# Kernel tuning notes

Measured on AMD Instinct MI355X. Metric: run time of the kernel, lower is better.

## Reference

```python
import jax, jax.numpy as jnp
import numpy as np

N, D_IN, D_OUT, E, H = 2048, 1024, 256, 50, 256  # tokens, input_dim, output_dim, edge_nodes, expert hidden
RH = 512  # distributed_processor hidden


def setup_inputs() -> dict:
    key = jax.random.key(0)
    ks = jax.random.split(key, 16)
    w = lambda k, shape: jax.random.normal(k, shape, jnp.float32) * 0.02
    z = lambda *shape: jnp.zeros(shape, jnp.float32)
    return {
        "x": jax.random.normal(ks[0], (N, D_IN), jnp.float32),
        # 50 expert MLPs: Linear(D_IN,H)-ReLU-Linear(H,D_OUT), stacked over E
        "ew1": w(ks[1], (E, D_IN, H)), "eb1": z(E, H),
        "ew2": w(ks[2], (E, H, D_OUT)), "eb2": z(E, D_OUT),
        # distributed_processor: Linear(E*D_OUT,RH)-ReLU-Linear(RH,D_OUT)
        "dw1": w(ks[3], (E * D_OUT, RH)), "db1": z(RH),
        "dw2": w(ks[4], (RH, D_OUT)), "db2": z(D_OUT),
        # latency_optimizer: Linear(D_IN,256)-ReLU-Linear(256,1)-Sigmoid
        "lw1": w(ks[5], (D_IN, 256)), "lb1": z(256),
        "lw2": w(ks[6], (256, 1)), "lb2": z(1),
        # bandwidth_optimizer: same structure
        "bw1": w(ks[7], (D_IN, 256)), "bb1": z(256),
        "bw2": w(ks[8], (256, 1)), "bb2": z(1),
        # privacy_preserver: Linear(D_OUT,256)-ReLU-Linear(256,D_OUT)
        "pw1": w(ks[9], (D_OUT, 256)), "pb1": z(256),
        "pw2": w(ks[10], (256, D_OUT)), "pb2": z(D_OUT),
    }


def reference(x, ew1, eb1, ew2, eb2, dw1, db1, dw2, db2,
              lw1, lb1, lw2, lb2, bw1, bb1, bw2, bb2,
              pw1, pb1, pw2, pb2):
    n = x.shape[0]
    # grouped expert MLPs (replaces the Python for-loop over edge nodes)
    h = jax.nn.relu(jnp.einsum('ni,eih->neh', x, ew1) + eb1)        # [N,E,H]
    expert_out = jnp.einsum('neh,eho->neo', h, ew2) + eb2           # [N,E,D_OUT]
    cat = expert_out.reshape(n, E * D_OUT)                          # torch.cat(dim=-1)
    # distributed_processor reduce
    dist = jax.nn.relu(cat @ dw1 + db1) @ dw2 + db2                 # [N,D_OUT]
    # gating scalars
    lat = jax.nn.sigmoid(jax.nn.relu(x @ lw1 + lb1) @ lw2 + lb2)    # [N,1]
    bwd = jax.nn.sigmoid(jax.nn.relu(x @ bw1 + bb1) @ bw2 + bb2)    # [N,1]
    # privacy_preserver
    priv = jax.nn.relu(dist @ pw1 + pb1) @ pw2 + pb2                # [N,D_OUT]
    return priv * lat * bwd
```

## Files before the change

kernel.cpp:

```cpp
#include <hip/hip_runtime.h>
#include <hip/hip_bf16.h>

typedef unsigned short u16;
typedef __attribute__((ext_vector_type(8))) __bf16 v8bf;
typedef __attribute__((ext_vector_type(4))) float v4f;

#define DEVINL __device__ __forceinline__

DEVINL u16 f2bf(float f) {
  union { float f; unsigned u; } v; v.f = f;
  unsigned u = v.u;
  return (u16)((u + 0x7FFFu + ((u >> 16) & 1u)) >> 16);
}
DEVINL float bf2f(u16 b) {
  union { unsigned u; float f; } v; v.u = ((unsigned)b) << 16;
  return v.f;
}

DEVINL void async16(const void* g, void* l) {
  __builtin_amdgcn_global_load_lds(
      (__attribute__((address_space(1))) void*)(g),
      (__attribute__((address_space(3))) void*)(l), 16, 0, 0);
}

DEVINL void f2b_body(const float* __restrict__ src, u16* __restrict__ dst, int base) {
  int i = base + threadIdx.x * 4;
  float4 v = *(const float4*)(src + i);
  unsigned lo = (unsigned)f2bf(v.x) | ((unsigned)f2bf(v.y) << 16);
  unsigned hi = (unsigned)f2bf(v.z) | ((unsigned)f2bf(v.w) << 16);
  uint2 o; o.x = lo; o.y = hi;
  *(uint2*)(dst + i) = o;
}

DEVINL void tr64(u16 (*t)[66], const float* __restrict__ src,
                 u16* __restrict__ dst, int R, int C, int bx, int by) {
  int r0 = by * 64, c0 = bx * 64;
  int tx = threadIdx.x & 15, ty = threadIdx.x >> 4;
#pragma unroll
  for (int i = 0; i < 4; ++i) {
    int rr = ty + i * 16;
    float4 v = *(const float4*)(src + (long)(r0 + rr) * C + c0 + tx * 4);
    u16* d = &t[rr][tx * 4];
    d[0] = f2bf(v.x); d[1] = f2bf(v.y); d[2] = f2bf(v.z); d[3] = f2bf(v.w);
  }
  __syncthreads();
#pragma unroll
  for (int i = 0; i < 4; ++i) {
    int cc = ty + i * 16;
    ushort4 o;
    o.x = t[tx * 4 + 0][cc]; o.y = t[tx * 4 + 1][cc];
    o.z = t[tx * 4 + 2][cc]; o.w = t[tx * 4 + 3][cc];
    *(ushort4*)(dst + (long)(c0 + cc) * R + r0 + tx * 4) = o;
  }
}

__global__ __launch_bounds__(256) void k_prep(
    const float* __restrict__ x, const float* __restrict__ ew2,
    const float* __restrict__ ew1, const float* __restrict__ dw1,
    const float* __restrict__ dw2, const float* __restrict__ lw1,
    const float* __restrict__ bw1, const float* __restrict__ pw1,
    const float* __restrict__ pw2,
    const float* __restrict__ eb1, const float* __restrict__ lb1,
    const float* __restrict__ bb1,
    u16* __restrict__ xb, u16* __restrict__ ew2b, u16* __restrict__ ew1tf,
    u16* __restrict__ dw1t, u16* __restrict__ dw2t,
    u16* __restrict__ pw1t, u16* __restrict__ pw2t,
    float* __restrict__ ebcat) {
  __shared__ u16 tile[64][66];
  int b = blockIdx.x;
  if (b < 2048) { f2b_body(x, xb, b * 1024); return; }
  b -= 2048;
  if (b < 3200) { f2b_body(ew2, ew2b, b * 1024); return; }
  b -= 3200;
  if (b < 3200) {
    int e = b >> 6, t = b & 63;
    tr64(tile, ew1 + (long)e * 1024 * 256, ew1tf + (long)e * 256 * 1024,
         1024, 256, t & 3, t >> 2);
    return;
  }
  b -= 3200;
  if (b < 1600) {
    tr64(tile, dw1, dw1t, 12800, 512, b & 7, b >> 3);
    return;
  }
  b -= 1600;
  if (b < 32) {
    tr64(tile, dw2, dw2t, 512, 256, b & 3, b >> 2);
    return;
  }
  b -= 32;
  if (b < 64) {
    tr64(tile, lw1, ew1tf + (long)12800 * 1024, 1024, 256, b & 3, b >> 2);
    return;
  }
  b -= 64;
  if (b < 64) {
    tr64(tile, bw1, ew1tf + (long)13056 * 1024, 1024, 256, b & 3, b >> 2);
    return;
  }
  b -= 64;
  if (b < 16) {
    tr64(tile, pw1, pw1t, 256, 256, b & 3, b >> 2);
    return;
  }
  b -= 16;
  if (b < 16) {
    tr64(tile, pw2, pw2t, 256, 256, b & 3, b >> 2);
    return;
  }
  b -= 16;
  {
    int i = b * 256 + threadIdx.x;
    float v;
    if (i < 12800) v = eb1[i];
    else if (i < 13056) v = lb1[i - 12800];
    else v = bb1[i - 13056];
    ebcat[i] = v;
  }
}

DEVINL void gemm128_body(u16* __restrict__ sA, u16* __restrict__ sB,
    int bx, int by, int z,
    const u16* __restrict__ A, int lda, long aBatch,
    const u16* __restrict__ B, int ldb, long bBatch,
    void* __restrict__ Cp, int ldc, long cBatch,
    int K,
    const float* __restrict__ bias, long biasBatch,
    const float* __restrict__ rowscale, int flags) {
  const int tid = threadIdx.x;
  const int w = tid >> 6, l = tid & 63;
  const u16* Ab = A + (long)z * aBatch + (long)by * 128 * lda;
  const u16* Bb = B + (long)z * bBatch + (long)bx * 128 * ldb;
  const int ldaB = lda * 2, ldbB = ldb * 2;
  const int wm = w >> 1, wn = w & 1;
  const int r = l & 15, kq = l >> 4;

  const int f0 = w * 1024 + l * 16;
  const int f1 = f0 + 4096;
  const int row0 = f0 >> 6, cb0 = f0 & 63;
  const int row1 = f1 >> 6, cb1 = f1 & 63;
  const int seg0 = w * 1024, seg1 = seg0 + 4096;

  v4f acc[4][4];
#pragma unroll
  for (int m = 0; m < 4; ++m)
#pragma unroll
    for (int n = 0; n < 4; ++n) acc[m][n] = v4f{0.f, 0.f, 0.f, 0.f};

  const char* gA = (const char*)Ab;
  const char* gB = (const char*)Bb;
  const int nkt = K / 32;

  async16(gA + (long)row0 * ldaB + cb0, (char*)sA + seg0);
  async16(gA + (long)row1 * ldaB + cb1, (char*)sA + seg1);
  async16(gB + (long)row0 * ldbB + cb0, (char*)sB + seg0);
  async16(gB + (long)row1 * ldbB + cb1, (char*)sB + seg1);
  __syncthreads();

  for (int kt = 0; kt < nkt; ++kt) {
    const int cur = kt & 1;
    if (kt + 1 < nkt) {
      const long ko = (long)(kt + 1) * 64;
      async16(gA + ko + (long)row0 * ldaB + cb0, (char*)sA + (cur ^ 1) * 8192 + seg0);
      async16(gA + ko + (long)row1 * ldaB + cb1, (char*)sA + (cur ^ 1) * 8192 + seg1);
      async16(gB + ko + (long)row0 * ldbB + cb0, (char*)sB + (cur ^ 1) * 8192 + seg0);
      async16(gB + ko + (long)row1 * ldbB + cb1, (char*)sB + (cur ^ 1) * 8192 + seg1);
    }
    v8bf af[4], bfr[4];
#pragma unroll
    for (int m = 0; m < 4; ++m)
      af[m] = *(const v8bf*)&sA[cur * 4096 + (wm * 64 + m * 16 + r) * 32 + kq * 8];
#pragma unroll
    for (int n = 0; n < 4; ++n)
      bfr[n] = *(const v8bf*)&sB[cur * 4096 + (wn * 64 + n * 16 + r) * 32 + kq * 8];
#pragma unroll
    for (int m = 0; m < 4; ++m)
#pragma unroll
      for (int n = 0; n < 4; ++n)
        acc[m][n] = __builtin_amdgcn_mfma_f32_16x16x32_bf16(af[m], bfr[n], acc[m][n], 0, 0, 0);
    __syncthreads();
  }

  const float* bz = bias ? (bias + (long)z * biasBatch) : nullptr;
  const long rowBase = (long)by * 128 + wm * 64 + kq * 4;
  const int colBase = bx * 128 + wn * 64 + r;
  float* Cf = (float*)Cp + (long)z * cBatch;
  u16* Ch = (u16*)Cp + (long)z * cBatch;
#pragma unroll
  for (int m = 0; m < 4; ++m) {
#pragma unroll
    for (int n = 0; n < 4; ++n) {
      const int col = colBase + n * 16;
      const float bv = bz ? bz[col] : 0.f;
#pragma unroll
      for (int i = 0; i < 4; ++i) {
        const long row = rowBase + m * 16 + i;
        float v = acc[m][n][i] + bv;
        if (flags & 1) v = fmaxf(v, 0.f);
        if (rowscale) v *= rowscale[row];
        const long idx = row * ldc + col;
        if (flags & 2) Cf[idx] = v;
        else Ch[idx] = f2bf(v);
      }
    }
  }
}

__global__ __launch_bounds__(256) void k_gemm(
    const u16* __restrict__ A, int lda, long aBatch,
    const u16* __restrict__ B, int ldb, long bBatch,
    void* __restrict__ Cp, int ldc, long cBatch,
    int K,
    const float* __restrict__ bias, long biasBatch,
    const float* __restrict__ rowscale, int flags) {
  __shared__ __align__(16) u16 sA[2 * 4096];
  __shared__ __align__(16) u16 sB[2 * 4096];
  gemm128_body(sA, sB, blockIdx.x, blockIdx.y, blockIdx.z,
               A, lda, aBatch, B, ldb, bBatch, Cp, ldc, cBatch, K,
               bias, biasBatch, rowscale, flags);
}

__global__ __launch_bounds__(256) void k_wft_bias(
    const u16* __restrict__ dw1t, const u16* __restrict__ ew2b,
    u16* __restrict__ Wft,
    const float* __restrict__ eb2, const float* __restrict__ db1,
    float* __restrict__ biasf) {
  __shared__ __align__(16) u16 sA[2 * 4096];
  __shared__ __align__(16) u16 sB[2 * 4096];
  int b = blockIdx.x;
  if (b < 512) {
    const u16* row = dw1t + (long)b * 12800;
    float s = 0.f;
    for (int c = threadIdx.x; c < 1600; c += 256) {
      ushort4 a0 = *(const ushort4*)(row + c * 8);
      ushort4 a1 = *(const ushort4*)(row + c * 8 + 4);
      float4 e0 = *(const float4*)(eb2 + c * 8);
      float4 e1 = *(const float4*)(eb2 + c * 8 + 4);
      s += bf2f(a0.x) * e0.x + bf2f(a0.y) * e0.y + bf2f(a0.z) * e0.z + bf2f(a0.w) * e0.w
         + bf2f(a1.x) * e1.x + bf2f(a1.y) * e1.y + bf2f(a1.z) * e1.z + bf2f(a1.w) * e1.w;
    }
    float* red = (float*)sA;
    red[threadIdx.x] = s;
    __syncthreads();
    for (int off = 128; off > 0; off >>= 1) {
      if (threadIdx.x < off) red[threadIdx.x] += red[threadIdx.x + off];
      __syncthreads();
    }
    if (threadIdx.x == 0) biasf[b] = red[0] + db1[b];
    return;
  }
  b -= 512;
  int bx = b & 1, by = (b >> 1) & 3, z = b >> 3;
  gemm128_body(sA, sB, bx, by, z,
               dw1t, 12800, 256, ew2b, 256, (long)256 * 256,
               Wft, 12800, 256, 256, nullptr, 0, nullptr, 0);
}

#define LDS_T(buf, op) (smem + ((buf) * 2 + (op)) * 16384)

#define READ_A(buf, mh) do {                                                   \
  const char* _t = (const char*)LDS_T(buf, 0);                                 \
  _Pragma("unroll") for (int m = 0; m < 4; ++m)                                \
    _Pragma("unroll") for (int kk = 0; kk < 2; ++kk)                           \
      a[m][kk] = *(const v8bf*)(_t +                                           \
        (wm * 128 + (mh) * 64 + m * 16 + r15) * 128 +                          \
        ((kk * 64 + kq * 16) ^ (swr << 4)));                                   \
} while (0)

#define READ_B(buf, nh, br) do {                                               \
  const char* _t = (const char*)LDS_T(buf, 1);                                 \
  _Pragma("unroll") for (int n = 0; n < 2; ++n)                                \
    _Pragma("unroll") for (int kk = 0; kk < 2; ++kk)                           \
      br[n][kk] = *(const v8bf*)(_t +                                          \
        (wn * 64 + (nh) * 32 + n * 16 + r15) * 128 +                          \
        ((kk * 64 + kq * 16) ^ (swr << 4)));                                   \
} while (0)

#define MMA(mh, nh, br) do {                                                   \
  _Pragma("unroll") for (int kk = 0; kk < 2; ++kk)                             \
    _Pragma("unroll") for (int m = 0; m < 4; ++m)                              \
      _Pragma("unroll") for (int n = 0; n < 2; ++n)                            \
        acc[(mh) * 4 + m][(nh) * 2 + n] =                                      \
          __builtin_amdgcn_mfma_f32_16x16x32_bf16(                             \
            a[m][kk], br[n][kk], acc[(mh) * 4 + m][(nh) * 2 + n], 0, 0, 0);    \
} while (0)

#define BAR() __builtin_amdgcn_s_barrier()
#define PRIO1() __builtin_amdgcn_s_setprio(1)
#define PRIO0() __builtin_amdgcn_s_setprio(0)
#define VM6() asm volatile("s_waitcnt vmcnt(6)" ::: "memory")
#define VM0() asm volatile("s_waitcnt vmcnt(0)" ::: "memory")
#define LGKM0() asm volatile("s_waitcnt lgkmcnt(0)" ::: "memory")

__global__ __launch_bounds__(512, 2) void k_gemm256(
    const u16* __restrict__ A, int lda, long aBatch,
    const u16* __restrict__ B, int ldb, long bBatch,
    void* __restrict__ Cp, int ldc, long cBatch,
    int K, int NX,
    const float* __restrict__ bias,
    const float* __restrict__ rowscale, int flags) {
  __shared__ __align__(16) u16 smem[2 * 2 * 16384];

  const int lin = blockIdx.x;
  const int idx = (lin & 7) * NX + (lin >> 3);
  const int by = idx & 7, bx = idx >> 3;

  const int tid = threadIdx.x;
  const int w = tid >> 6, l = tid & 63;
  const int wm = w >> 2, wn = w & 3;
  const int r15 = l & 15, kq = l >> 4, swr = l & 7;
  const int z = blockIdx.z;

  const int rl = l >> 3;
  const int scol = ((l & 7) ^ rl) << 4;

  const long ldaB = (long)lda * 2, ldbB = (long)ldb * 2;
  const char* gAs = (const char*)(A + (long)z * aBatch) +
                    ((long)by * 256 + rl) * ldaB + scol;
  const char* gBs = (const char*)(B + (long)z * bBatch) +
                    ((long)bx * 256 + rl) * ldbB + scol;

  auto stA = [&](int buf, int R0, int kt) {
    async16(gAs + (long)R0 * ldaB + (long)kt * 128, (char*)LDS_T(buf, 0) + R0 * 128);
  };
  auto stB = [&](int buf, int R0, int kt) {
    async16(gBs + (long)R0 * ldbB + (long)kt * 128, (char*)LDS_T(buf, 1) + R0 * 128);
  };
  auto stAU0 = [&](int buf, int kt) { stA(buf, w * 8, kt);       stA(buf, 128 + w * 8, kt); };
  auto stAU1 = [&](int buf, int kt) { stA(buf, 64 + w * 8, kt);  stA(buf, 192 + w * 8, kt); };
  auto stBU0 = [&](int buf, int kt) { int R = (w >> 1) * 64 + (w & 1) * 16;      stB(buf, R, kt); stB(buf, R + 8, kt); };
  auto stBU1 = [&](int buf, int kt) { int R = (w >> 1) * 64 + (w & 1) * 16 + 32; stB(buf, R, kt); stB(buf, R + 8, kt); };

  v4f acc[8][4];
#pragma unroll
  for (int m = 0; m < 8; ++m)
#pragma unroll
    for (int n = 0; n < 4; ++n) acc[m][n] = v4f{0.f, 0.f, 0.f, 0.f};
  v8bf a[4][2], b0[2][2], b1[2][2];

  const int NT = K >> 6;
  const int NI = (NT >> 1) - 1;

  stAU0(0, 0); stBU0(0, 0); stBU1(0, 0); stAU1(0, 0);
  stAU0(1, 1); stBU0(1, 1); stBU1(1, 1);
  VM6();
  BAR();

  int kt0 = 0;
  for (int i = 0; i < NI; ++i, kt0 += 2) {
    READ_A(0, 0); READ_B(0, 0, b0);
    stAU1(1, kt0 + 1);
    BAR(); LGKM0(); PRIO1(); MMA(0, 0, b0); PRIO0(); BAR();
    READ_B(0, 1, b1);
    stAU0(0, kt0 + 2);
    BAR(); LGKM0(); PRIO1(); MMA(0, 1, b1); PRIO0(); BAR();
    READ_A(0, 1);
    stBU0(0, kt0 + 2);
    BAR(); LGKM0(); PRIO1(); MMA(1, 1, b1); PRIO0(); BAR();
    stBU1(0, kt0 + 2);
    BAR(); PRIO1(); MMA(1, 0, b0); PRIO0(); VM6(); BAR();
    READ_A(1, 0); READ_B(1, 0, b0);
    stAU1(0, kt0 + 2);
    BAR(); LGKM0(); PRIO1(); MMA(0, 0, b0); PRIO0(); BAR();
    READ_B(1, 1, b1);
    stAU0(1, kt0 + 3);
    BAR(); LGKM0(); PRIO1(); MMA(0, 1, b1); PRIO0(); BAR();
    READ_A(1, 1);
    stBU0(1, kt0 + 3);
    BAR(); LGKM0(); PRIO1(); MMA(1, 1, b1); PRIO0(); BAR();
    stBU1(1, kt0 + 3);
    BAR(); PRIO1(); MMA(1, 0, b0); PRIO0(); VM6(); BAR();
  }

  READ_A(0, 0); READ_B(0, 0, b0);
  stAU1(1, kt0 + 1);
  BAR(); LGKM0(); PRIO1(); MMA(0, 0, b0); PRIO0(); BAR();
  READ_B(0, 1, b1);
  BAR(); LGKM0(); PRIO1(); MMA(0, 1, b1); PRIO0(); BAR();
  READ_A(0, 1);
  BAR(); LGKM0(); PRIO1(); MMA(1, 1, b1); PRIO0(); BAR();
  BAR(); PRIO1(); MMA(1, 0, b0); PRIO0(); VM0(); BAR();
  READ_A(1, 0); READ_B(1, 0, b0);
  BAR(); LGKM0(); PRIO1(); MMA(0, 0, b0); PRIO0(); BAR();
  READ_B(1, 1, b1);
  BAR(); LGKM0(); PRIO1(); MMA(0, 1, b1); PRIO0(); BAR();
  READ_A(1, 1);
  BAR(); LGKM0(); PRIO1(); MMA(1, 1, b1); PRIO0(); BAR();
  PRIO1(); MMA(1, 0, b0); PRIO0();

  const long rowBase = (long)by * 256 + wm * 128 + kq * 4;
  const int colBase = bx * 256 + wn * 64 + r15;
  float* Cf = (float*)Cp + (long)z * cBatch;
  u16* Ch = (u16*)Cp + (long)z * cBatch;
#pragma unroll
  for (int mf = 0; mf < 8; ++mf) {
#pragma unroll
    for (int nf = 0; nf < 4; ++nf) {
      const int col = colBase + nf * 16;
      const float bv = bias ? bias[col] : 0.f;
#pragma unroll
      for (int j = 0; j < 4; ++j) {
        const long row = rowBase + mf * 16 + j;
        float v = acc[mf][nf][j] + bv;
        if (flags & 1) v = fmaxf(v, 0.f);
        if (rowscale) v *= rowscale[row];
        const long idx = row * ldc + col;
        if (flags & 2) Cf[idx] = v;
        else Ch[idx] = f2bf(v);
      }
    }
  }
}

__global__ __launch_bounds__(256) void k_tail(
    const float* __restrict__ part,
    const float* __restrict__ biasf,
    const u16* __restrict__ hg,
    const float* __restrict__ lw2, const float* __restrict__ lb2,
    const float* __restrict__ bw2, const float* __restrict__ bb2,
    const u16* __restrict__ dw2t,
    const float* __restrict__ db2,
    const u16* __restrict__ pw1t,
    const float* __restrict__ pb1,
    const u16* __restrict__ pw2t,
    const float* __restrict__ pb2,
    float* __restrict__ out) {
  __shared__ __align__(16) u16 dhs[16][520];
  __shared__ __align__(16) u16 ds2[16][264];
  __shared__ __align__(16) u16 phs[16][264];
  __shared__ float gl[16];
  const int tid = threadIdx.x;
  const int w = tid >> 6, l = tid & 63;
  const int r = l & 15, kq = l >> 4;
  const int r0 = blockIdx.x * 16;

#pragma unroll
  for (int i = 0; i < 8; ++i) {
    int e = (i * 256 + tid) * 4;
    int row = e >> 9, col = e & 511;
    const float* pp = part + (long)(r0 + row) * 512 + col;
    float4 s = *(const float4*)pp;
#pragma unroll
    for (int k = 1; k < 8; ++k) {
      float4 t = *(const float4*)(pp + (long)k * (2048 * 512));
      s.x += t.x; s.y += t.y; s.z += t.z; s.w += t.w;
    }
    float4 bv = *(const float4*)(biasf + col);
    ushort4 o;
    o.x = f2bf(fmaxf(s.x + bv.x, 0.f));
    o.y = f2bf(fmaxf(s.y + bv.y, 0.f));
    o.z = f2bf(fmaxf(s.z + bv.z, 0.f));
    o.w = f2bf(fmaxf(s.w + bv.w, 0.f));
    *(ushort4*)&dhs[row][col] = o;
  }

#pragma unroll
  for (int j = 0; j < 4; ++j) {
    int rr = w * 4 + j;
    const u16* rowp = hg + (long)(r0 + rr) * 13312;
    float sa = 0.f, sb = 0.f;
#pragma unroll
    for (int jj = 0; jj < 4; ++jj) {
      int i = l * 4 + jj;
      sa += bf2f(rowp[i]) * lw2[i];
      sb += bf2f(rowp[256 + i]) * bw2[i];
    }
#pragma unroll
    for (int off = 32; off > 0; off >>= 1) {
      sa += __shfl_down(sa, off, 64);
      sb += __shfl_down(sb, off, 64);
    }
    if (l == 0) {
      float ga = 1.f / (1.f + expf(-(sa + lb2[0])));
      float gb = 1.f / (1.f + expf(-(sb + bb2[0])));
      gl[rr] = ga * gb;
    }
  }
  __syncthreads();

  v4f acc[4];
#pragma unroll
  for (int n = 0; n < 4; ++n) acc[n] = v4f{0.f, 0.f, 0.f, 0.f};
#pragma unroll 4
  for (int kt = 0; kt < 16; ++kt) {
    v8bf af = *(const v8bf*)&dhs[r][kt * 32 + kq * 8];
#pragma unroll
    for (int n = 0; n < 4; ++n) {
      v8bf bf = *(const v8bf*)(dw2t + (long)(w * 64 + n * 16 + r) * 512 + kt * 32 + kq * 8);
      acc[n] = __builtin_amdgcn_mfma_f32_16x16x32_bf16(af, bf, acc[n], 0, 0, 0);
    }
  }
#pragma unroll
  for (int n = 0; n < 4; ++n) {
    int col = w * 64 + n * 16 + r;
    float bv = db2[col];
#pragma unroll
    for (int j = 0; j < 4; ++j) ds2[kq * 4 + j][col] = f2bf(acc[n][j] + bv);
  }
  __syncthreads();

#pragma unroll
  for (int n = 0; n < 4; ++n) acc[n] = v4f{0.f, 0.f, 0.f, 0.f};
#pragma unroll 4
  for (int kt = 0; kt < 8; ++kt) {
    v8bf af = *(const v8bf*)&ds2[r][kt * 32 + kq * 8];
#pragma unroll
    for (int n = 0; n < 4; ++n) {
      v8bf bf = *(const v8bf*)(pw1t + (long)(w * 64 + n * 16 + r) * 256 + kt * 32 + kq * 8);
      acc[n] = __builtin_amdgcn_mfma_f32_16x16x32_bf16(af, bf, acc[n], 0, 0, 0);
    }
  }
#pragma unroll
  for (int n = 0; n < 4; ++n) {
    int col = w * 64 + n * 16 + r;
    float bv = pb1[col];
#pragma unroll
    for (int j = 0; j < 4; ++j) phs[kq * 4 + j][col] = f2bf(fmaxf(acc[n][j] + bv, 0.f));
  }
  __syncthreads();

#pragma unroll
  for (int n = 0; n < 4; ++n) acc[n] = v4f{0.f, 0.f, 0.f, 0.f};
#pragma unroll 4
  for (int kt = 0; kt < 8; ++kt) {
    v8bf af = *(const v8bf*)&phs[r][kt * 32 + kq * 8];
#pragma unroll
    for (int n = 0; n < 4; ++n) {
      v8bf bf = *(const v8bf*)(pw2t + (long)(w * 64 + n * 16 + r) * 256 + kt * 32 + kq * 8);
      acc[n] = __builtin_amdgcn_mfma_f32_16x16x32_bf16(af, bf, acc[n], 0, 0, 0);
    }
  }
#pragma unroll
  for (int n = 0; n < 4; ++n) {
    int col = w * 64 + n * 16 + r;
    float bv = pb2[col];
#pragma unroll
    for (int j = 0; j < 4; ++j) {
      int row = kq * 4 + j;
      out[(long)(r0 + row) * 256 + col] = (acc[n][j] + bv) * gl[row];
    }
  }
}

extern "C" void kernel_launch(void* const* d_in, const int* in_sizes, int n_in,
                              void* d_out, int out_size, void* d_ws, size_t ws_size,
                              hipStream_t stream) {
  const float* x   = (const float*)d_in[0];
  const float* ew1 = (const float*)d_in[1];
  const float* eb1 = (const float*)d_in[2];
  const float* ew2 = (const float*)d_in[3];
  const float* eb2 = (const float*)d_in[4];
  const float* dw1 = (const float*)d_in[5];
  const float* db1 = (const float*)d_in[6];
  const float* dw2 = (const float*)d_in[7];
  const float* db2 = (const float*)d_in[8];
  const float* lw1 = (const float*)d_in[9];
  const float* lb1 = (const float*)d_in[10];
  const float* lw2 = (const float*)d_in[11];
  const float* lb2 = (const float*)d_in[12];
  const float* bw1 = (const float*)d_in[13];
  const float* bb1 = (const float*)d_in[14];
  const float* bw2 = (const float*)d_in[15];
  const float* bb2 = (const float*)d_in[16];
  const float* pw1 = (const float*)d_in[17];
  const float* pb1 = (const float*)d_in[18];
  const float* pw2 = (const float*)d_in[19];
  const float* pb2 = (const float*)d_in[20];

  const int S = 8, Ksplit = 1600;

  char* p = (char*)d_ws;
  auto alloc = [&](size_t bytes) {
    char* q = p;
    p += (bytes + 255) & ~(size_t)255;
    return q;
  };
  u16* xb      = (u16*)alloc((size_t)2048 * 1024 * 2);
  u16* ew1tf   = (u16*)alloc((size_t)13312 * 1024 * 2);
  u16* Wft     = (u16*)alloc((size_t)512 * 12800 * 2);
  u16* dw2t    = (u16*)alloc((size_t)256 * 512 * 2);
  u16* pw1t    = (u16*)alloc((size_t)256 * 256 * 2);
  u16* pw2t    = (u16*)alloc((size_t)256 * 256 * 2);
  float* ebcat = (float*)alloc(13312 * 4);
  float* biasf = (float*)alloc(512 * 4);
  float* part  = (float*)alloc((size_t)S * 2048 * 512 * 4);
  char* uni    = alloc((size_t)2048 * 13312 * 2);
  u16* h_all   = (u16*)uni;
  u16* ew2b    = (u16*)uni;
  u16* dw1t    = (u16*)(uni + (((size_t)50 * 256 * 256 * 2 + 255) & ~(size_t)255));
  (void)in_sizes; (void)n_in; (void)out_size; (void)ws_size;

  k_prep<<<dim3(10292), 256, 0, stream>>>(
      x, ew2, ew1, dw1, dw2, lw1, bw1, pw1, pw2, eb1, lb1, bb1,
      xb, ew2b, ew1tf, dw1t, dw2t, pw1t, pw2t, ebcat);

  k_wft_bias<<<dim3(912), 256, 0, stream>>>(dw1t, ew2b, Wft, eb2, db1, biasf);

  k_gemm256<<<dim3(416, 1, 1), 512, 0, stream>>>(
      xb, 1024, 0, ew1tf, 1024, 0, h_all, 13312, 0,
      1024, 52, ebcat, nullptr, 1);

  k_gemm<<<dim3(4, 16, S), 256, 0, stream>>>(
      h_all, 13312, Ksplit, Wft, 12800, Ksplit, part, 512, (long)2048 * 512,
      Ksplit, nullptr, 0, nullptr, 2);

  k_tail<<<dim3(128), 256, 0, stream>>>(
      part, biasf, h_all + 12800, lw2, lb2, bw2, bb2,
      dw2t, db2, pw1t, pb1, pw2t, pb2, (float*)d_out);
}
```

Before: 191.8 us.

## Fuse weight-fold and bias kernel into first expert GEMM launch

Folds the separate k_wft_bias launch into k_gemm256 as extra blocks, so the Wft fold GEMM and the bias reductions run alongside the main expert GEMM instead of as a serial step. Each 512-thread extra block runs two 256-thread sub-tasks, with both halves sharing one __syncthreads in the reduction path. Scratch buffers are remapped so ew2b/dw1t live in the split-K partial buffer rather than aliasing h_all, which the concurrent GEMM writes. This removes one launch and its tail, but adds heterogeneous blocks that compete for CUs with the main GEMM.

```diff
diff --git a/kernel.cpp b/kernel.cpp
--- a/kernel.cpp
+++ b/kernel.cpp
@@ -119,7 +119,7 @@
   }
 }
 
-DEVINL void gemm128_body(u16* __restrict__ sA, u16* __restrict__ sB,
+DEVINL void gemm128_body(int tid, u16* __restrict__ sA, u16* __restrict__ sB,
     int bx, int by, int z,
     const u16* __restrict__ A, int lda, long aBatch,
     const u16* __restrict__ B, int ldb, long bBatch,
@@ -127,7 +127,6 @@
     int K,
     const float* __restrict__ bias, long biasBatch,
     const float* __restrict__ rowscale, int flags) {
-  const int tid = threadIdx.x;
   const int w = tid >> 6, l = tid & 63;
   const u16* Ab = A + (long)z * aBatch + (long)by * 128 * lda;
   const u16* Bb = B + (long)z * bBatch + (long)bx * 128 * ldb;
@@ -215,46 +214,11 @@
     const float* __restrict__ rowscale, int flags) {
   __shared__ __align__(16) u16 sA[2 * 4096];
   __shared__ __align__(16) u16 sB[2 * 4096];
-  gemm128_body(sA, sB, blockIdx.x, blockIdx.y, blockIdx.z,
+  gemm128_body(threadIdx.x, sA, sB, blockIdx.x, blockIdx.y, blockIdx.z,
                A, lda, aBatch, B, ldb, bBatch, Cp, ldc, cBatch, K,
                bias, biasBatch, rowscale, flags);
 }
 
-__global__ __launch_bounds__(256) void k_wft_bias(
-    const u16* __restrict__ dw1t, const u16* __restrict__ ew2b,
-    u16* __restrict__ Wft,
-    const float* __restrict__ eb2, const float* __restrict__ db1,
-    float* __restrict__ biasf) {
-  __shared__ __align__(16) u16 sA[2 * 4096];
-  __shared__ __align__(16) u16 sB[2 * 4096];
-  int b = blockIdx.x;
-  if (b < 512) {
-    const u16* row = dw1t + (long)b * 12800;
-    float s = 0.f;
-    for (int c = threadIdx.x; c < 1600; c += 256) {
-      ushort4 a0 = *(const ushort4*)(row + c * 8);
-      ushort4 a1 = *(const ushort4*)(row + c * 8 + 4);
-      float4 e0 = *(const float4*)(eb2 + c * 8);
-      float4 e1 = *(const float4*)(eb2 + c * 8 + 4);
-      s += bf2f(a0.x) * e0.x + bf2f(a0.y) * e0.y + bf2f(a0.z) * e0.z + bf2f(a0.w) * e0.w
-         + bf2f(a1.x) * e1.x + bf2f(a1.y) * e1.y + bf2f(a1.z) * e1.z + bf2f(a1.w) * e1.w;
-    }
-    float* red = (float*)sA;
-    red[threadIdx.x] = s;
-    __syncthreads();
-    for (int off = 128; off > 0; off >>= 1) {
-      if (threadIdx.x < off) red[threadIdx.x] += red[threadIdx.x + off];
-      __syncthreads();
-    }
-    if (threadIdx.x == 0) biasf[b] = red[0] + db1[b];
-    return;
-  }
-  b -= 512;
-  int bx = b & 1, by = (b >> 1) & 3, z = b >> 3;
-  gemm128_body(sA, sB, bx, by, z,
-               dw1t, 12800, 256, ew2b, 256, (long)256 * 256,
-               Wft, 12800, 256, 256, nullptr, 0, nullptr, 0);
-}
 
 #define LDS_T(buf, op) (smem + ((buf) * 2 + (op)) * 16384)
 
@@ -293,32 +257,67 @@
 #define LGKM0() asm volatile("s_waitcnt lgkmcnt(0)" ::: "memory")
 
 __global__ __launch_bounds__(512, 2) void k_gemm256(
-    const u16* __restrict__ A, int lda, long aBatch,
-    const u16* __restrict__ B, int ldb, long bBatch,
-    void* __restrict__ Cp, int ldc, long cBatch,
+    const u16* __restrict__ A, int lda,
+    const u16* __restrict__ B, int ldb,
+    void* __restrict__ Cp, int ldc,
     int K, int NX,
-    const float* __restrict__ bias,
-    const float* __restrict__ rowscale, int flags) {
+    const float* __restrict__ bias, int flags,
+    const u16* __restrict__ dw1t, const u16* __restrict__ ew2b,
+    u16* __restrict__ Wft,
+    const float* __restrict__ eb2, const float* __restrict__ db1,
+    float* __restrict__ biasf, int ngemm1) {
   __shared__ __align__(16) u16 smem[2 * 2 * 16384];
 
   const int lin = blockIdx.x;
+  const int tid = threadIdx.x;
+
+  if (lin >= ngemm1) {
+    int fb = lin - ngemm1;
+    int sub = tid >> 8, t = tid & 255;
+    if (fb < 200) {
+      int tt = fb * 2 + sub;
+      int bx = tt & 1, by = (tt >> 1) & 3, z = tt >> 3;
+      u16* base = smem + sub * 16384;
+      gemm128_body(t, base, base + 8192, bx, by, z,
+                   dw1t, 12800, 256, ew2b, 256, (long)256 * 256,
+                   Wft, 12800, 256, 256, nullptr, 0, nullptr, 0);
+      return;
+    }
+    int r = (fb - 200) * 2 + sub;
+    const u16* row = dw1t + (long)r * 12800;
+    float s = 0.f;
+    for (int c = t; c < 1600; c += 256) {
+      ushort4 a0 = *(const ushort4*)(row + c * 8);
+      ushort4 a1 = *(const ushort4*)(row + c * 8 + 4);
+      float4 e0 = *(const float4*)(eb2 + c * 8);
+      float4 e1 = *(const float4*)(eb2 + c * 8 + 4);
+      s += bf2f(a0.x) * e0.x + bf2f(a0.y) * e0.y + bf2f(a0.z) * e0.z + bf2f(a0.w) * e0.w
+         + bf2f(a1.x) * e1.x + bf2f(a1.y) * e1.y + bf2f(a1.z) * e1.z + bf2f(a1.w) * e1.w;
+    }
+    float* red = (float*)smem + sub * 256;
+    red[t] = s;
+    __syncthreads();
+    for (int off = 128; off > 0; off >>= 1) {
+      if (t < off) red[t] += red[t + off];
+      __syncthreads();
+    }
+    if (t == 0) biasf[r] = red[0] + db1[r];
+    return;
+  }
+
   const int idx = (lin & 7) * NX + (lin >> 3);
   const int by = idx & 7, bx = idx >> 3;
 
-  const int tid = threadIdx.x;
   const int w = tid >> 6, l = tid & 63;
   const int wm = w >> 2, wn = w & 3;
   const int r15 = l & 15, kq = l >> 4, swr = l & 7;
-  const int z = blockIdx.z;
 
   const int rl = l >> 3;
   const int scol = ((l & 7) ^ rl) << 4;
 
   const long ldaB = (long)lda * 2, ldbB = (long)ldb * 2;
-  const char* gAs = (const char*)(A + (long)z * aBatch) +
-                    ((long)by * 256 + rl) * ldaB + scol;
-  const char* gBs = (const char*)(B + (long)z * bBatch) +
-                    ((long)bx * 256 + rl) * ldbB + scol;
+  const char* gAs = (const char*)A + ((long)by * 256 + rl) * ldaB + scol;
+  const char* gBs = (const char*)B + ((long)bx * 256 + rl) * ldbB + scol;
 
   auto stA = [&](int buf, int R0, int kt) {
     async16(gAs + (long)R0 * ldaB + (long)kt * 128, (char*)LDS_T(buf, 0) + R0 * 128);
@@ -390,8 +389,7 @@
 
   const long rowBase = (long)by * 256 + wm * 128 + kq * 4;
   const int colBase = bx * 256 + wn * 64 + r15;
-  float* Cf = (float*)Cp + (long)z * cBatch;
-  u16* Ch = (u16*)Cp + (long)z * cBatch;
+  u16* Ch = (u16*)Cp;
 #pragma unroll
   for (int mf = 0; mf < 8; ++mf) {
 #pragma unroll
@@ -403,10 +401,7 @@
         const long row = rowBase + mf * 16 + j;
         float v = acc[mf][nf][j] + bv;
         if (flags & 1) v = fmaxf(v, 0.f);
-        if (rowscale) v *= rowscale[row];
-        const long idx = row * ldc + col;
-        if (flags & 2) Cf[idx] = v;
-        else Ch[idx] = f2bf(v);
+        Ch[row * ldc + col] = f2bf(v);
       }
     }
   }
@@ -584,21 +579,19 @@
   float* ebcat = (float*)alloc(13312 * 4);
   float* biasf = (float*)alloc(512 * 4);
   float* part  = (float*)alloc((size_t)S * 2048 * 512 * 4);
-  char* uni    = alloc((size_t)2048 * 13312 * 2);
-  u16* h_all   = (u16*)uni;
-  u16* ew2b    = (u16*)uni;
-  u16* dw1t    = (u16*)(uni + (((size_t)50 * 256 * 256 * 2 + 255) & ~(size_t)255));
+  u16* h_all   = (u16*)alloc((size_t)2048 * 13312 * 2);
+  u16* ew2b    = (u16*)part;
+  u16* dw1t    = (u16*)((char*)part + (((size_t)50 * 256 * 256 * 2 + 255) & ~(size_t)255));
   (void)in_sizes; (void)n_in; (void)out_size; (void)ws_size;
 
   k_prep<<<dim3(10292), 256, 0, stream>>>(
       x, ew2, ew1, dw1, dw2, lw1, bw1, pw1, pw2, eb1, lb1, bb1,
       xb, ew2b, ew1tf, dw1t, dw2t, pw1t, pw2t, ebcat);
 
-  k_wft_bias<<<dim3(912), 256, 0, stream>>>(dw1t, ew2b, Wft, eb2, db1, biasf);
-
-  k_gemm256<<<dim3(416, 1, 1), 512, 0, stream>>>(
-      xb, 1024, 0, ew1tf, 1024, 0, h_all, 13312, 0,
-      1024, 52, ebcat, nullptr, 1);
+  k_gemm256<<<dim3(872, 1, 1), 512, 0, stream>>>(
+      xb, 1024, ew1tf, 1024, h_all, 13312,
+      1024, 52, ebcat, 1,
+      dw1t, ew2b, Wft, eb2, db1, biasf, 416);
 
   k_gemm<<<dim3(4, 16, S), 256, 0, stream>>>(
       h_all, 13312, Ksplit, Wft, 12800, Ksplit, part, 512, (long)2048 * 512,
```

Result: faster. 169.8 us (-11.5%).
